# Optimization experiments

Hardware: AMD Instinct MI355X
Metric: run time of the kernel (lower is better)

The kernel has to match this reference:

```python
import jax, jax.numpy as jnp
import numpy as np

B, S, E = 1, 2048, 4096
H, D = 32, 128  # num_heads, head_dim


def setup_inputs() -> dict:
    key = jax.random.key(0)
    k1, k2, k3 = jax.random.split(key, 3)
    hidden_states = jax.random.normal(k1, (B, S, E), dtype=jnp.float32)
    # real RoPE tables (half-rotation / llama-style), base 10000
    inv_freq = 1.0 / (10000.0 ** (np.arange(0, D, 2, dtype=np.float32) / D))  # [D/2]
    pos = np.arange(S, dtype=np.float32)
    freqs = np.outer(pos, inv_freq)                      # [S, D/2]
    emb = np.concatenate([freqs, freqs], axis=-1)        # [S, D]
    cos = jnp.asarray(np.cos(emb), dtype=jnp.float32)
    sin = jnp.asarray(np.sin(emb), dtype=jnp.float32)
    w_pack = jax.random.normal(k2, (3 * E, E), dtype=jnp.float32) * (E ** -0.5)
    w_o = jax.random.normal(k3, (E, E), dtype=jnp.float32) * (E ** -0.5)
    return {"hidden_states": hidden_states, "cos": cos, "sin": sin,
            "w_pack": w_pack, "w_o": w_o}


def _rotate_half(x):
    x1, x2 = jnp.split(x, 2, axis=-1)
    return jnp.concatenate([-x2, x1], axis=-1)


def reference(hidden_states, cos, sin, w_pack, w_o):
    # fused QKV projection (W_pack, no bias)
    qkv = jnp.einsum('bse,fe->bsf', hidden_states, w_pack)      # [B,S,3E]
    q, k, v = jnp.split(qkv, 3, axis=-1)
    q = q.reshape(B, S, H, D)
    k = k.reshape(B, S, H, D)
    v = v.reshape(B, S, H, D)
    # RoPE (7B path; is_13b=False)
    c = cos[None, :, None, :]
    s = sin[None, :, None, :]
    q = q * c + _rotate_half(q) * s
    k = k * c + _rotate_half(k) * s
    # causal attention (prefill, empty past KV cache)
    scale = 1.0 / jnp.sqrt(jnp.asarray(D, dtype=q.dtype))
    scores = jnp.einsum('bqhd,bkhd->bhqk', q, k) * scale        # [B,H,S,S]
    causal = jnp.tril(jnp.ones((S, S), dtype=bool))
    scores = jnp.where(causal[None, None], scores, jnp.asarray(-1e30, scores.dtype))
    probs = jax.nn.softmax(scores, axis=-1)
    attn = jnp.einsum('bhqk,bkhd->bqhd', probs, v)              # [B,S,H,D]
    attn = attn.reshape(B, S, H * D)
    # output projection
    return jnp.einsum('bsf,ef->bse', attn, w_o)
```

## Files before the change

### kernel.cpp

```cpp
#include <hip/hip_runtime.h>

typedef unsigned short u16;
typedef unsigned int   u32;
typedef __attribute__((ext_vector_type(8))) short short8;
typedef __attribute__((ext_vector_type(4))) float f32x4;

__device__ __forceinline__ float b2f(u16 u) {
  union { float f; u32 i; } v; v.i = ((u32)u) << 16; return v.f;
}
__device__ __forceinline__ u16 f2b(float f) {
  union { float f; u32 i; } v; v.f = f;
  u32 r = v.i + 0x7fffu + ((v.i >> 16) & 1u);
  return (u16)(r >> 16);
}

__device__ __forceinline__ void gload_lds16(const void* g, void* l) {
  __builtin_amdgcn_global_load_lds(
      (const __attribute__((address_space(1))) void*)g,
      (__attribute__((address_space(3))) void*)l, 16, 0, 0);
}

template <int N> __device__ __forceinline__ void wait_vmcnt() {
  if constexpr (N == 0)      asm volatile("s_waitcnt vmcnt(0)" ::: "memory");
  else if constexpr (N == 2) asm volatile("s_waitcnt vmcnt(2)" ::: "memory");
  else if constexpr (N == 3) asm volatile("s_waitcnt vmcnt(3)" ::: "memory");
  else if constexpr (N == 6) asm volatile("s_waitcnt vmcnt(6)" ::: "memory");
  else if constexpr (N == 8) asm volatile("s_waitcnt vmcnt(8)" ::: "memory");
  else static_assert(N < 0, "unsupported vmcnt literal");
}

__device__ __forceinline__ ushort4 cvt4(float4 v) {
  ushort4 o;
  o.x = f2b(v.x); o.y = f2b(v.y); o.z = f2b(v.z); o.w = f2b(v.w);
  return o;
}

__global__ __launch_bounds__(256) void cvt_all(const float* __restrict__ hs,
                                               const float* __restrict__ wp,
                                               const float* __restrict__ wo,
                                               u16* __restrict__ h_bf,
                                               u16* __restrict__ wp_bf,
                                               u16* __restrict__ wo_bf) {
  const long H4 = 2097152, W4 = 12582912, O4 = 4194304;
  for (long i = (long)blockIdx.x * 256 + threadIdx.x; i < H4 + W4 + O4;
       i += (long)gridDim.x * 256) {
    if (i < H4)
      ((ushort4*)h_bf)[i] = cvt4(((const float4*)hs)[i]);
    else if (i < H4 + W4)
      ((ushort4*)wp_bf)[i - H4] = cvt4(((const float4*)wp)[i - H4]);
    else
      ((ushort4*)wo_bf)[i - H4 - W4] = cvt4(((const float4*)wo)[i - H4 - W4]);
  }
}

__device__ __forceinline__ short8 frag_ld64(const u16* base, int rbase, int kk,
                                            int fr, int fq) {
  const int r = rbase + fr;
  return *(const short8*)(base + r * 64 + ((((kk << 2) + fq) ^ (r & 7)) << 3));
}

__global__ __launch_bounds__(512, 2) void gemm8p(const u16* __restrict__ A,
                                                 const u16* __restrict__ B,
                                                 u16* __restrict__ Cq,
                                                 u16* __restrict__ VT,
                                                 int M, int N, int K) {
  constexpr int AE = 16384;
  constexpr int BUFSZ = AE + 12288;
  __shared__ u16 lds[2 * BUFSZ];
  const int tid = threadIdx.x;
  const int wid = tid >> 6, lane = tid & 63;
  const int fr = lane & 15, fq = lane >> 4;
  const int mA = (wid >> 2) * 128;
  const int nB = (wid & 3) * 48;

  const int nty = M >> 8;
  const int qx = gridDim.x >> 3;
  const int wg = (blockIdx.x & 7) * qx + (blockIdx.x >> 3);
  const int by = wg % nty, bx = wg / nty;
  const long row0 = (long)by * 256, col0 = (long)bx * 192;

  const int rr8 = tid >> 3;
  const int jl = (tid & 7) ^ (rr8 & 7);
  const u16* gA = A + (row0 + rr8) * (long)K + jl * 8;
  const u16* gB = B + (col0 + rr8) * (long)K + jl * 8;

  f32x4 acc[8][3];
#pragma unroll
  for (int m = 0; m < 8; ++m)
#pragma unroll
    for (int n = 0; n < 3; ++n) acc[m][n] = f32x4{0.f, 0.f, 0.f, 0.f};

  const int NT = K >> 6;

  auto stageA = [&](int i, int t) {
    gload_lds16(gA + (long)(i * 64) * K + (long)t * 64,
                lds + (t & 1) * BUFSZ + (i * 512 + tid) * 8);
  };
  auto stageB = [&](int i, int t) {
    gload_lds16(gB + (long)(i * 64) * K + (long)t * 64,
                lds + (t & 1) * BUFSZ + AE + (i * 512 + tid) * 8);
  };

#pragma unroll
  for (int i = 0; i < 4; ++i) stageA(i, 0);
#pragma unroll
  for (int i = 0; i < 3; ++i) stageB(i, 0);
#pragma unroll
  for (int i = 0; i < 3; ++i) stageB(i, 1);
  wait_vmcnt<3>();
  __builtin_amdgcn_s_barrier();

  for (int t = 0; t < NT; ++t) {
    const u16* SA = lds + (t & 1) * BUFSZ;
    const u16* SB = SA + AE;
    short8 a0[4], a1[4], b0[3], b1[3];

#pragma unroll
    for (int m = 0; m < 4; ++m) a0[m] = frag_ld64(SA, mA + m * 16, 0, fr, fq);
#pragma unroll
    for (int n = 0; n < 3; ++n) b0[n] = frag_ld64(SB, nB + n * 16, 0, fr, fq);
#pragma unroll
    for (int n = 0; n < 3; ++n) b1[n] = frag_ld64(SB, nB + n * 16, 1, fr, fq);
    if (t + 1 < NT) { stageA(0, t + 1); stageA(1, t + 1); }
    __builtin_amdgcn_s_setprio(1);
#pragma unroll
    for (int m = 0; m < 4; ++m)
#pragma unroll
      for (int n = 0; n < 3; ++n)
        acc[m][n] = __builtin_amdgcn_mfma_f32_16x16x32_bf16(a0[m], b0[n], acc[m][n], 0, 0, 0);
    __builtin_amdgcn_s_setprio(0);
    asm volatile("s_waitcnt lgkmcnt(0)" ::: "memory");
    __builtin_amdgcn_s_barrier();

#pragma unroll
    for (int m = 0; m < 4; ++m) a1[m] = frag_ld64(SA, mA + 64 + m * 16, 0, fr, fq);
    if (t + 1 < NT) { stageA(2, t + 1); stageA(3, t + 1); }
    __builtin_amdgcn_s_setprio(1);
#pragma unroll
    for (int m = 0; m < 4; ++m)
#pragma unroll
      for (int n = 0; n < 3; ++n)
        acc[4 + m][n] = __builtin_amdgcn_mfma_f32_16x16x32_bf16(a1[m], b0[n], acc[4 + m][n], 0, 0, 0);
    __builtin_amdgcn_s_setprio(0);
    __builtin_amdgcn_s_barrier();

#pragma unroll
    for (int m = 0; m < 4; ++m) a0[m] = frag_ld64(SA, mA + m * 16, 1, fr, fq);
    if (t + 2 < NT) { stageB(0, t + 2); stageB(1, t + 2); }
    __builtin_amdgcn_s_setprio(1);
#pragma unroll
    for (int m = 0; m < 4; ++m)
#pragma unroll
      for (int n = 0; n < 3; ++n)
        acc[m][n] = __builtin_amdgcn_mfma_f32_16x16x32_bf16(a0[m], b1[n], acc[m][n], 0, 0, 0);
    __builtin_amdgcn_s_setprio(0);
    __builtin_amdgcn_s_barrier();

#pragma unroll
    for (int m = 0; m < 4; ++m) a1[m] = frag_ld64(SA, mA + 64 + m * 16, 1, fr, fq);
    if (t + 2 < NT) stageB(2, t + 2);
    __builtin_amdgcn_s_setprio(1);
#pragma unroll
    for (int m = 0; m < 4; ++m)
#pragma unroll
      for (int n = 0; n < 3; ++n)
        acc[4 + m][n] = __builtin_amdgcn_mfma_f32_16x16x32_bf16(a1[m], b1[n], acc[4 + m][n], 0, 0, 0);
    __builtin_amdgcn_s_setprio(0);
    if (t + 2 < NT) wait_vmcnt<3>();
    else            wait_vmcnt<0>();
    __builtin_amdgcn_s_barrier();
  }

#pragma unroll
  for (int m = 0; m < 8; ++m)
#pragma unroll
    for (int n = 0; n < 3; ++n) {
      const long c = col0 + nB + n * 16 + fr;
      const long rb = row0 + mA + m * 16 + fq * 4;
      if (c >= 8192) {
        ushort4 o;
        o.x = f2b(acc[m][n][0]); o.y = f2b(acc[m][n][1]);
        o.z = f2b(acc[m][n][2]); o.w = f2b(acc[m][n][3]);
        *(ushort4*)(VT + (c - 8192) * 2048 + rb) = o;
      } else {
#pragma unroll
        for (int j = 0; j < 4; ++j) Cq[(rb + j) * N + c] = f2b(acc[m][n][j]);
      }
    }
}

__global__ __launch_bounds__(512, 2) void gemm2_4p(const u16* __restrict__ A,
                                                   const u16* __restrict__ B,
                                                   float* __restrict__ C,
                                                   int M, int N, int K) {
  constexpr int AE = 16384;
  constexpr int BUFSZ = AE + 8192;
  __shared__ u16 lds[2 * BUFSZ];
  const int tid = threadIdx.x;
  const int wid = tid >> 6, lane = tid & 63;
  const int fr = lane & 15, fq = lane >> 4;
  const int mA = (wid >> 2) * 128;
  const int nB = (wid & 3) * 32;

  const int nty = M >> 8;
  const int qx = gridDim.x >> 3;
  const int wg = (blockIdx.x & 7) * qx + (blockIdx.x >> 3);
  const int by = wg % nty, bx = wg / nty;
  const long row0 = (long)by * 256, col0 = (long)bx * 128;

  const int rr8 = tid >> 3;
  const int jl = (tid & 7) ^ (rr8 & 7);
  const u16* gA = A + (row0 + rr8) * (long)K + jl * 8;
  const u16* gB = B + (col0 + rr8) * (long)K + jl * 8;

  f32x4 acc[8][2];
#pragma unroll
  for (int m = 0; m < 8; ++m)
#pragma unroll
    for (int n = 0; n < 2; ++n) acc[m][n] = f32x4{0.f, 0.f, 0.f, 0.f};

  const int NT = K >> 6;

  auto stageA = [&](int i, int t) {
    gload_lds16(gA + (long)(i * 64) * K + (long)t * 64,
                lds + (t & 1) * BUFSZ + (i * 512 + tid) * 8);
  };
  auto stageB = [&](int i, int t) {
    gload_lds16(gB + (long)(i * 64) * K + (long)t * 64,
                lds + (t & 1) * BUFSZ + AE + (i * 512 + tid) * 8);
  };

#pragma unroll
  for (int i = 0; i < 4; ++i) stageA(i, 0);
#pragma unroll
  for (int i = 0; i < 2; ++i) stageB(i, 0);
#pragma unroll
  for (int i = 0; i < 2; ++i) stageB(i, 1);
  wait_vmcnt<2>();
  __builtin_amdgcn_s_barrier();

  for (int t = 0; t < NT; ++t) {
    const u16* SA = lds + (t & 1) * BUFSZ;
    const u16* SB = SA + AE;
    short8 a0[4], a1[4], b0[2], b1[2];

#pragma unroll
    for (int m = 0; m < 4; ++m) a0[m] = frag_ld64(SA, mA + m * 16, 0, fr, fq);
#pragma unroll
    for (int n = 0; n < 2; ++n) b0[n] = frag_ld64(SB, nB + n * 16, 0, fr, fq);
#pragma unroll
    for (int n = 0; n < 2; ++n) b1[n] = frag_ld64(SB, nB + n * 16, 1, fr, fq);
    if (t + 1 < NT) { stageA(0, t + 1); stageA(1, t + 1); }
    __builtin_amdgcn_s_setprio(1);
#pragma unroll
    for (int m = 0; m < 4; ++m)
#pragma unroll
      for (int n = 0; n < 2; ++n)
        acc[m][n] = __builtin_amdgcn_mfma_f32_16x16x32_bf16(a0[m], b0[n], acc[m][n], 0, 0, 0);
    __builtin_amdgcn_s_setprio(0);
    asm volatile("s_waitcnt lgkmcnt(0)" ::: "memory");
    __builtin_amdgcn_s_barrier();

#pragma unroll
    for (int m = 0; m < 4; ++m) a1[m] = frag_ld64(SA, mA + 64 + m * 16, 0, fr, fq);
    if (t + 1 < NT) { stageA(2, t + 1); stageA(3, t + 1); }
    __builtin_amdgcn_s_setprio(1);
#pragma unroll
    for (int m = 0; m < 4; ++m)
#pragma unroll
      for (int n = 0; n < 2; ++n)
        acc[4 + m][n] = __builtin_amdgcn_mfma_f32_16x16x32_bf16(a1[m], b0[n], acc[4 + m][n], 0, 0, 0);
    __builtin_amdgcn_s_setprio(0);
    __builtin_amdgcn_s_barrier();

#pragma unroll
    for (int m = 0; m < 4; ++m) a0[m] = frag_ld64(SA, mA + m * 16, 1, fr, fq);
    if (t + 2 < NT) stageB(0, t + 2);
    __builtin_amdgcn_s_setprio(1);
#pragma unroll
    for (int m = 0; m < 4; ++m)
#pragma unroll
      for (int n = 0; n < 2; ++n)
        acc[m][n] = __builtin_amdgcn_mfma_f32_16x16x32_bf16(a0[m], b1[n], acc[m][n], 0, 0, 0);
    __builtin_amdgcn_s_setprio(0);
    __builtin_amdgcn_s_barrier();

#pragma unroll
    for (int m = 0; m < 4; ++m) a1[m] = frag_ld64(SA, mA + 64 + m * 16, 1, fr, fq);
    if (t + 2 < NT) stageB(1, t + 2);
    __builtin_amdgcn_s_setprio(1);
#pragma unroll
    for (int m = 0; m < 4; ++m)
#pragma unroll
      for (int n = 0; n < 2; ++n)
        acc[4 + m][n] = __builtin_amdgcn_mfma_f32_16x16x32_bf16(a1[m], b1[n], acc[4 + m][n], 0, 0, 0);
    __builtin_amdgcn_s_setprio(0);
    if (t + 2 < NT) wait_vmcnt<2>();
    else            wait_vmcnt<0>();
    __builtin_amdgcn_s_barrier();
  }

#pragma unroll
  for (int m = 0; m < 8; ++m)
#pragma unroll
    for (int n = 0; n < 2; ++n)
#pragma unroll
      for (int j = 0; j < 4; ++j) {
        const long r = row0 + mA + m * 16 + fq * 4 + j;
        const long c = col0 + nB + n * 16 + fr;
        C[r * N + c] = acc[m][n][j];
      }
}

__global__ __launch_bounds__(256) void rope_qk(u16* __restrict__ qkv,
                                               const float* __restrict__ cosb,
                                               const float* __restrict__ sinb) {
  const int idx = blockIdx.x * 256 + threadIdx.x;
  const int dq  = idx & 15;
  const int h   = (idx >> 4) & 31;
  const int seg = (idx >> 9) & 1;
  const int s   = idx >> 10;
  const int d0  = dq * 4;
  u16* base = qkv + (long)s * 12288 + seg * 4096 + h * 128;
  const ushort4 x1 = *(const ushort4*)(base + d0);
  const ushort4 x2 = *(const ushort4*)(base + d0 + 64);
  const float4 c1 = *(const float4*)(cosb + s * 128 + d0);
  const float4 s1 = *(const float4*)(sinb + s * 128 + d0);
  const float4 c2 = *(const float4*)(cosb + s * 128 + d0 + 64);
  const float4 s2 = *(const float4*)(sinb + s * 128 + d0 + 64);
  const float scale = seg ? 1.0f : 0.08838834764831845f;
  float x1f[4] = {b2f(x1.x), b2f(x1.y), b2f(x1.z), b2f(x1.w)};
  float x2f[4] = {b2f(x2.x), b2f(x2.y), b2f(x2.z), b2f(x2.w)};
  const float c1a[4] = {c1.x, c1.y, c1.z, c1.w}, s1a[4] = {s1.x, s1.y, s1.z, s1.w};
  const float c2a[4] = {c2.x, c2.y, c2.z, c2.w}, s2a[4] = {s2.x, s2.y, s2.z, s2.w};
  ushort4 o1, o2;
  u16* o1p = (u16*)&o1; u16* o2p = (u16*)&o2;
#pragma unroll
  for (int j = 0; j < 4; ++j) {
    o1p[j] = f2b((x1f[j] * c1a[j] - x2f[j] * s1a[j]) * scale);
    o2p[j] = f2b((x2f[j] * c2a[j] + x1f[j] * s2a[j]) * scale);
  }
  *(ushort4*)(base + d0) = o1;
  *(ushort4*)(base + d0 + 64) = o2;
}

__global__ __launch_bounds__(256) void attn_fwd(const u16* __restrict__ Qb,
                                                const u16* __restrict__ Kb,
                                                const u16* __restrict__ Vt,
                                                u16* __restrict__ Ob) {
  const int h = blockIdx.y;
  const int tid = threadIdx.x;
  const int wid = tid >> 6, lane = tid & 63;
  const int fr = lane & 15, fq = lane >> 4;

  __shared__ u16 Ks[3][64 * 128];
  __shared__ u16 Vts[3][128 * 64];
  __shared__ u16 Ps[4][32 * 72];

  auto stage = [&](int t, int buf) {
    const int kv0 = t * 64;
#pragma unroll
    for (int i = 0; i < 4; ++i) {
      const int c = wid * 4 + i;
      {
        const int r = c * 4 + (lane >> 4);
        const int p = lane & 15;
        const int jsrc = p ^ (r & 7);
        gload_lds16(Kb + (long)(kv0 + r) * 12288 + h * 128 + jsrc * 8,
                    (char*)Ks[buf] + c * 1024);
      }
      {
        const int d = c * 8 + (lane >> 3);
        const int p = lane & 7;
        const int jsrc = p ^ (d & 7);
        gload_lds16(Vt + (long)(h * 128 + d) * 2048 + kv0 + jsrc * 8,
                    (char*)Vts[buf] + c * 1024);
      }
    }
  };

#pragma unroll
  for (int pass = 0; pass < 2; ++pass) {
    const int qt = pass == 0 ? (int)blockIdx.x : 15 - (int)blockIdx.x;
    const int q0 = qt * 128;
    const int nt = 2 * qt + 2;
    const int wq_hi = q0 + wid * 32 + 31;

    short8 qf[2][4];
#pragma unroll
    for (int m = 0; m < 2; ++m) {
      const long qrow = q0 + wid * 32 + m * 16 + fr;
#pragma unroll
      for (int kk = 0; kk < 4; ++kk)
        qf[m][kk] = *(const short8*)(Qb + qrow * 12288 + h * 128 + kk * 32 + fq * 8);
    }

    f32x4 Oacc[2][8];
#pragma unroll
    for (int m = 0; m < 2; ++m)
#pragma unroll
      for (int f = 0; f < 8; ++f) Oacc[m][f] = f32x4{0.f, 0.f, 0.f, 0.f};
    float mrun[2][4], lrun[2][4];
#pragma unroll
    for (int m = 0; m < 2; ++m)
#pragma unroll
      for (int j = 0; j < 4; ++j) { mrun[m][j] = -1e30f; lrun[m][j] = 0.f; }

    stage(0, 0);
    if (nt > 1) { stage(1, 1); wait_vmcnt<8>(); }
    else        wait_vmcnt<0>();
    __builtin_amdgcn_s_barrier();

    for (int t = 0; t < nt; ++t) {
      const int cur = t % 3;
      const int kv0 = t * 64;
      if (t + 2 < nt) stage(t + 2, (t + 2) % 3);

      if (kv0 <= wq_hi) {
        f32x4 S[2][4];
#pragma unroll
        for (int m = 0; m < 2; ++m)
#pragma unroll
          for (int n = 0; n < 4; ++n) S[m][n] = f32x4{0.f, 0.f, 0.f, 0.f};
#pragma unroll
        for (int kk = 0; kk < 4; ++kk) {
          short8 kf[4];
#pragma unroll
          for (int n = 0; n < 4; ++n) {
            const int r = n * 16 + fr;
            const int p = (kk * 4 + fq) ^ (r & 7);
            kf[n] = *(const short8*)((const char*)Ks[cur] + r * 256 + p * 16);
          }
#pragma unroll
          for (int m = 0; m < 2; ++m)
#pragma unroll
            for (int n = 0; n < 4; ++n)
              S[m][n] = __builtin_amdgcn_mfma_f32_16x16x32_bf16(qf[m][kk], kf[n], S[m][n], 0, 0, 0);
        }

        float P[2][4][4];
#pragma unroll
        for (int m = 0; m < 2; ++m) {
          float tm[4] = {-1e30f, -1e30f, -1e30f, -1e30f};
#pragma unroll
          for (int n = 0; n < 4; ++n) {
            const int kv = kv0 + n * 16 + fr;
#pragma unroll
            for (int j = 0; j < 4; ++j) {
              const int qi = q0 + wid * 32 + m * 16 + fq * 4 + j;
              const float s = (kv <= qi) ? S[m][n][j] : -1e30f;
              P[m][n][j] = s;
              tm[j] = fmaxf(tm[j], s);
            }
          }
#pragma unroll
          for (int j = 0; j < 4; ++j)
#pragma unroll
            for (int msk = 1; msk < 16; msk <<= 1)
              tm[j] = fmaxf(tm[j], __shfl_xor(tm[j], msk));

          float al[4], rs[4];
#pragma unroll
          for (int j = 0; j < 4; ++j) {
            const float mn = fmaxf(mrun[m][j], tm[j]);
            al[j] = __expf(mrun[m][j] - mn);
            mrun[m][j] = mn;
            rs[j] = 0.f;
          }
#pragma unroll
          for (int n = 0; n < 4; ++n)
#pragma unroll
            for (int j = 0; j < 4; ++j) {
              const float p = __expf(P[m][n][j] - mrun[m][j]);
              P[m][n][j] = p;
              rs[j] += p;
            }
#pragma unroll
          for (int j = 0; j < 4; ++j) {
#pragma unroll
            for (int msk = 1; msk < 16; msk <<= 1) rs[j] += __shfl_xor(rs[j], msk);
            lrun[m][j] = lrun[m][j] * al[j] + rs[j];
          }
#pragma unroll
          for (int f = 0; f < 8; ++f) {
            f32x4 o = Oacc[m][f];
#pragma unroll
            for (int j = 0; j < 4; ++j) o[j] *= al[j];
            Oacc[m][f] = o;
          }
        }

#pragma unroll
        for (int m = 0; m < 2; ++m)
#pragma unroll
          for (int n = 0; n < 4; ++n)
#pragma unroll
            for (int j = 0; j < 4; ++j)
              Ps[wid][(m * 16 + fq * 4 + j) * 72 + n * 16 + fr] = f2b(P[m][n][j]);

#pragma unroll
        for (int kb = 0; kb < 2; ++kb) {
          short8 pa0 = *(const short8*)(Ps[wid] + (fr) * 72 + kb * 32 + fq * 8);
          short8 pa1 = *(const short8*)(Ps[wid] + (16 + fr) * 72 + kb * 32 + fq * 8);
#pragma unroll
          for (int f = 0; f < 8; ++f) {
            const int d = f * 16 + fr;
            const int p = (kb * 4 + fq) ^ (d & 7);
            short8 vf = *(const short8*)((const char*)Vts[cur] + d * 128 + p * 16);
            Oacc[0][f] = __builtin_amdgcn_mfma_f32_16x16x32_bf16(pa0, vf, Oacc[0][f], 0, 0, 0);
            Oacc[1][f] = __builtin_amdgcn_mfma_f32_16x16x32_bf16(pa1, vf, Oacc[1][f], 0, 0, 0);
          }
        }
      }
      if (t + 2 < nt) wait_vmcnt<8>();
      else            wait_vmcnt<0>();
      __builtin_amdgcn_s_barrier();
    }

#pragma unroll
    for (int m = 0; m < 2; ++m)
#pragma unroll
      for (int j = 0; j < 4; ++j) {
        const float inv = 1.f / lrun[m][j];
        const long r = q0 + wid * 32 + m * 16 + fq * 4 + j;
#pragma unroll
        for (int f = 0; f < 8; ++f)
          Ob[r * 4096 + h * 128 + f * 16 + fr] = f2b(Oacc[m][f][j] * inv);
      }
  }
}

extern "C" void kernel_launch(void* const* d_in, const int* in_sizes, int n_in,
                              void* d_out, int out_size, void* d_ws, size_t ws_size,
                              hipStream_t stream) {
  const float* hs   = (const float*)d_in[0];
  const float* cosb = (const float*)d_in[1];
  const float* sinb = (const float*)d_in[2];
  const float* wp   = (const float*)d_in[3];
  const float* wo   = (const float*)d_in[4];
  float* out = (float*)d_out;
  char* ws = (char*)d_ws;

  u16* h_bf  = (u16*)(ws);
  u16* attn  = (u16*)(ws);
  u16* wp_bf = (u16*)(ws + 16777216);
  u16* wo_bf = (u16*)(ws + 117440512);
  u16* qkv   = (u16*)(ws + 150994944);
  u16* vt    = (u16*)(ws + 201326592);

  cvt_all<<<4096, 256, 0, stream>>>(hs, wp, wo, h_bf, wp_bf, wo_bf);
  gemm8p<<<512, 512, 0, stream>>>(h_bf, wp_bf, qkv, vt, 2048, 12288, 4096);
  rope_qk<<<8192, 256, 0, stream>>>(qkv, cosb, sinb);
  attn_fwd<<<dim3(8, 32), 256, 0, stream>>>(qkv, qkv + 4096, vt, attn);
  gemm2_4p<<<256, 512, 0, stream>>>(attn, wo_bf, out, 2048, 4096, 4096);
}
```

Baseline: 467.1 us.

## Process two adjacent query tiles per 512-thread attention block with shared K/V staging

The attention kernel moves from 4 waves running two load-balanced q-tile passes one after another to 8 waves in two groups. Each group handles one of two adjacent q-tiles at the same time, and both groups share the same K/V LDS tiles. This halves K/V staging traffic per tile and raises waves per CU for latency hiding. In exchange the per-block work now grows with blockIdx.x, so the old pair balancing (tile i with tile 15-i) is lost. The pipeline also drops from triple to double buffering with a full vmcnt(0) wait on every step, which shortens the prefetch distance.

```diff
diff --git a/kernel.cpp b/kernel.cpp
--- a/kernel.cpp
+++ b/kernel.cpp
@@ -25,7 +25,6 @@
   else if constexpr (N == 2) asm volatile("s_waitcnt vmcnt(2)" ::: "memory");
   else if constexpr (N == 3) asm volatile("s_waitcnt vmcnt(3)" ::: "memory");
   else if constexpr (N == 6) asm volatile("s_waitcnt vmcnt(6)" ::: "memory");
-  else if constexpr (N == 8) asm volatile("s_waitcnt vmcnt(8)" ::: "memory");
   else static_assert(N < 0, "unsupported vmcnt literal");
 }
 
@@ -344,24 +343,26 @@
   *(ushort4*)(base + d0 + 64) = o2;
 }
 
-__global__ __launch_bounds__(256) void attn_fwd(const u16* __restrict__ Qb,
-                                                const u16* __restrict__ Kb,
-                                                const u16* __restrict__ Vt,
-                                                u16* __restrict__ Ob) {
+__global__ __launch_bounds__(512, 2) void attn_fwd(const u16* __restrict__ Qb,
+                                                   const u16* __restrict__ Kb,
+                                                   const u16* __restrict__ Vt,
+                                                   u16* __restrict__ Ob) {
   const int h = blockIdx.y;
   const int tid = threadIdx.x;
   const int wid = tid >> 6, lane = tid & 63;
+  const int grp = wid >> 2;
+  const int w4 = wid & 3;
   const int fr = lane & 15, fq = lane >> 4;
 
-  __shared__ u16 Ks[3][64 * 128];
-  __shared__ u16 Vts[3][128 * 64];
-  __shared__ u16 Ps[4][32 * 72];
+  __shared__ u16 Ks[2][64 * 128];
+  __shared__ u16 Vts[2][128 * 64];
+  __shared__ u16 Ps[8][32 * 72];
 
   auto stage = [&](int t, int buf) {
     const int kv0 = t * 64;
 #pragma unroll
-    for (int i = 0; i < 4; ++i) {
-      const int c = wid * 4 + i;
+    for (int i = 0; i < 2; ++i) {
+      const int c = wid * 2 + i;
       {
         const int r = c * 4 + (lane >> 4);
         const int p = lane & 15;
@@ -379,155 +380,150 @@
     }
   };
 
-#pragma unroll
-  for (int pass = 0; pass < 2; ++pass) {
-    const int qt = pass == 0 ? (int)blockIdx.x : 15 - (int)blockIdx.x;
-    const int q0 = qt * 128;
-    const int nt = 2 * qt + 2;
-    const int wq_hi = q0 + wid * 32 + 31;
-
-    short8 qf[2][4];
-#pragma unroll
-    for (int m = 0; m < 2; ++m) {
-      const long qrow = q0 + wid * 32 + m * 16 + fr;
-#pragma unroll
-      for (int kk = 0; kk < 4; ++kk)
-        qf[m][kk] = *(const short8*)(Qb + qrow * 12288 + h * 128 + kk * 32 + fq * 8);
-    }
-
-    f32x4 Oacc[2][8];
-#pragma unroll
-    for (int m = 0; m < 2; ++m)
-#pragma unroll
-      for (int f = 0; f < 8; ++f) Oacc[m][f] = f32x4{0.f, 0.f, 0.f, 0.f};
-    float mrun[2][4], lrun[2][4];
-#pragma unroll
-    for (int m = 0; m < 2; ++m)
-#pragma unroll
-      for (int j = 0; j < 4; ++j) { mrun[m][j] = -1e30f; lrun[m][j] = 0.f; }
-
-    stage(0, 0);
-    if (nt > 1) { stage(1, 1); wait_vmcnt<8>(); }
-    else        wait_vmcnt<0>();
-    __builtin_amdgcn_s_barrier();
-
-    for (int t = 0; t < nt; ++t) {
-      const int cur = t % 3;
-      const int kv0 = t * 64;
-      if (t + 2 < nt) stage(t + 2, (t + 2) % 3);
-
-      if (kv0 <= wq_hi) {
-        f32x4 S[2][4];
+  const int qt = 2 * (int)blockIdx.x + (grp ^ 1);
+  const int q0 = qt * 128;
+  const int nt = 4 * (int)blockIdx.x + 4;
+  const int wq_hi = q0 + w4 * 32 + 31;
+
+  short8 qf[2][4];
+#pragma unroll
+  for (int m = 0; m < 2; ++m) {
+    const long qrow = q0 + w4 * 32 + m * 16 + fr;
+#pragma unroll
+    for (int kk = 0; kk < 4; ++kk)
+      qf[m][kk] = *(const short8*)(Qb + qrow * 12288 + h * 128 + kk * 32 + fq * 8);
+  }
+
+  f32x4 Oacc[2][8];
+#pragma unroll
+  for (int m = 0; m < 2; ++m)
+#pragma unroll
+    for (int f = 0; f < 8; ++f) Oacc[m][f] = f32x4{0.f, 0.f, 0.f, 0.f};
+  float mrun[2][4], lrun[2][4];
+#pragma unroll
+  for (int m = 0; m < 2; ++m)
+#pragma unroll
+    for (int j = 0; j < 4; ++j) { mrun[m][j] = -1e30f; lrun[m][j] = 0.f; }
+
+  stage(0, 0);
+  wait_vmcnt<0>();
+  __builtin_amdgcn_s_barrier();
+
+  for (int t = 0; t < nt; ++t) {
+    const int cur = t & 1;
+    const int kv0 = t * 64;
+    if (t + 1 < nt) stage(t + 1, cur ^ 1);
+
+    if (kv0 <= wq_hi) {
+      f32x4 S[2][4];
+#pragma unroll
+      for (int m = 0; m < 2; ++m)
+#pragma unroll
+        for (int n = 0; n < 4; ++n) S[m][n] = f32x4{0.f, 0.f, 0.f, 0.f};
+#pragma unroll
+      for (int kk = 0; kk < 4; ++kk) {
+        short8 kf[4];
+#pragma unroll
+        for (int n = 0; n < 4; ++n) {
+          const int r = n * 16 + fr;
+          const int p = (kk * 4 + fq) ^ (r & 7);
+          kf[n] = *(const short8*)((const char*)Ks[cur] + r * 256 + p * 16);
+        }
 #pragma unroll
         for (int m = 0; m < 2; ++m)
 #pragma unroll
-          for (int n = 0; n < 4; ++n) S[m][n] = f32x4{0.f, 0.f, 0.f, 0.f};
-#pragma unroll
-        for (int kk = 0; kk < 4; ++kk) {
-          short8 kf[4];
-#pragma unroll
-          for (int n = 0; n < 4; ++n) {
-            const int r = n * 16 + fr;
-            const int p = (kk * 4 + fq) ^ (r & 7);
-            kf[n] = *(const short8*)((const char*)Ks[cur] + r * 256 + p * 16);
-          }
-#pragma unroll
-          for (int m = 0; m < 2; ++m)
-#pragma unroll
-            for (int n = 0; n < 4; ++n)
-              S[m][n] = __builtin_amdgcn_mfma_f32_16x16x32_bf16(qf[m][kk], kf[n], S[m][n], 0, 0, 0);
-        }
-
-        float P[2][4][4];
-#pragma unroll
-        for (int m = 0; m < 2; ++m) {
-          float tm[4] = {-1e30f, -1e30f, -1e30f, -1e30f};
-#pragma unroll
-          for (int n = 0; n < 4; ++n) {
-            const int kv = kv0 + n * 16 + fr;
-#pragma unroll
-            for (int j = 0; j < 4; ++j) {
-              const int qi = q0 + wid * 32 + m * 16 + fq * 4 + j;
-              const float s = (kv <= qi) ? S[m][n][j] : -1e30f;
-              P[m][n][j] = s;
-              tm[j] = fmaxf(tm[j], s);
-            }
-          }
-#pragma unroll
-          for (int j = 0; j < 4; ++j)
-#pragma unroll
-            for (int msk = 1; msk < 16; msk <<= 1)
-              tm[j] = fmaxf(tm[j], __shfl_xor(tm[j], msk));
-
-          float al[4], rs[4];
+          for (int n = 0; n < 4; ++n)
+            S[m][n] = __builtin_amdgcn_mfma_f32_16x16x32_bf16(qf[m][kk], kf[n], S[m][n], 0, 0, 0);
+      }
+
+      float P[2][4][4];
+#pragma unroll
+      for (int m = 0; m < 2; ++m) {
+        float tm[4] = {-1e30f, -1e30f, -1e30f, -1e30f};
+#pragma unroll
+        for (int n = 0; n < 4; ++n) {
+          const int kv = kv0 + n * 16 + fr;
 #pragma unroll
           for (int j = 0; j < 4; ++j) {
-            const float mn = fmaxf(mrun[m][j], tm[j]);
-            al[j] = __expf(mrun[m][j] - mn);
-            mrun[m][j] = mn;
-            rs[j] = 0.f;
-          }
-#pragma unroll
-          for (int n = 0; n < 4; ++n)
-#pragma unroll
-            for (int j = 0; j < 4; ++j) {
-              const float p = __expf(P[m][n][j] - mrun[m][j]);
-              P[m][n][j] = p;
-              rs[j] += p;
-            }
-#pragma unroll
-          for (int j = 0; j < 4; ++j) {
-#pragma unroll
-            for (int msk = 1; msk < 16; msk <<= 1) rs[j] += __shfl_xor(rs[j], msk);
-            lrun[m][j] = lrun[m][j] * al[j] + rs[j];
-          }
-#pragma unroll
-          for (int f = 0; f < 8; ++f) {
-            f32x4 o = Oacc[m][f];
-#pragma unroll
-            for (int j = 0; j < 4; ++j) o[j] *= al[j];
-            Oacc[m][f] = o;
+            const int qi = q0 + w4 * 32 + m * 16 + fq * 4 + j;
+            const float s = (kv <= qi) ? S[m][n][j] : -1e30f;
+            P[m][n][j] = s;
+            tm[j] = fmaxf(tm[j], s);
           }
         }
-
-#pragma unroll
-        for (int m = 0; m < 2; ++m)
-#pragma unroll
-          for (int n = 0; n < 4; ++n)
-#pragma unroll
-            for (int j = 0; j < 4; ++j)
-              Ps[wid][(m * 16 + fq * 4 + j) * 72 + n * 16 + fr] = f2b(P[m][n][j]);
-
-#pragma unroll
-        for (int kb = 0; kb < 2; ++kb) {
-          short8 pa0 = *(const short8*)(Ps[wid] + (fr) * 72 + kb * 32 + fq * 8);
-          short8 pa1 = *(const short8*)(Ps[wid] + (16 + fr) * 72 + kb * 32 + fq * 8);
-#pragma unroll
-          for (int f = 0; f < 8; ++f) {
-            const int d = f * 16 + fr;
-            const int p = (kb * 4 + fq) ^ (d & 7);
-            short8 vf = *(const short8*)((const char*)Vts[cur] + d * 128 + p * 16);
-            Oacc[0][f] = __builtin_amdgcn_mfma_f32_16x16x32_bf16(pa0, vf, Oacc[0][f], 0, 0, 0);
-            Oacc[1][f] = __builtin_amdgcn_mfma_f32_16x16x32_bf16(pa1, vf, Oacc[1][f], 0, 0, 0);
+#pragma unroll
+        for (int j = 0; j < 4; ++j)
+#pragma unroll
+          for (int msk = 1; msk < 16; msk <<= 1)
+            tm[j] = fmaxf(tm[j], __shfl_xor(tm[j], msk));
+
+        float al[4], rs[4];
+#pragma unroll
+        for (int j = 0; j < 4; ++j) {
+          const float mn = fmaxf(mrun[m][j], tm[j]);
+          al[j] = __expf(mrun[m][j] - mn);
+          mrun[m][j] = mn;
+          rs[j] = 0.f;
+        }
+#pragma unroll
+        for (int n = 0; n < 4; ++n)
+#pragma unroll
+          for (int j = 0; j < 4; ++j) {
+            const float p = __expf(P[m][n][j] - mrun[m][j]);
+            P[m][n][j] = p;
+            rs[j] += p;
           }
+#pragma unroll
+        for (int j = 0; j < 4; ++j) {
+#pragma unroll
+          for (int msk = 1; msk < 16; msk <<= 1) rs[j] += __shfl_xor(rs[j], msk);
+          lrun[m][j] = lrun[m][j] * al[j] + rs[j];
         }
-      }
-      if (t + 2 < nt) wait_vmcnt<8>();
-      else            wait_vmcnt<0>();
-      __builtin_amdgcn_s_barrier();
+#pragma unroll
+        for (int f = 0; f < 8; ++f) {
+          f32x4 o = Oacc[m][f];
+#pragma unroll
+          for (int j = 0; j < 4; ++j) o[j] *= al[j];
+          Oacc[m][f] = o;
+        }
+      }
+
+#pragma unroll
+      for (int m = 0; m < 2; ++m)
+#pragma unroll
+        for (int n = 0; n < 4; ++n)
+#pragma unroll
+          for (int j = 0; j < 4; ++j)
+            Ps[wid][(m * 16 + fq * 4 + j) * 72 + n * 16 + fr] = f2b(P[m][n][j]);
+
+#pragma unroll
+      for (int kb = 0; kb < 2; ++kb) {
+        short8 pa0 = *(const short8*)(Ps[wid] + (fr) * 72 + kb * 32 + fq * 8);
+        short8 pa1 = *(const short8*)(Ps[wid] + (16 + fr) * 72 + kb * 32 + fq * 8);
+#pragma unroll
+        for (int f = 0; f < 8; ++f) {
+          const int d = f * 16 + fr;
+          const int p = (kb * 4 + fq) ^ (d & 7);
+          short8 vf = *(const short8*)((const char*)Vts[cur] + d * 128 + p * 16);
+          Oacc[0][f] = __builtin_amdgcn_mfma_f32_16x16x32_bf16(pa0, vf, Oacc[0][f], 0, 0, 0);
+          Oacc[1][f] = __builtin_amdgcn_mfma_f32_16x16x32_bf16(pa1, vf, Oacc[1][f], 0, 0, 0);
+        }
+      }
     }
-
-#pragma unroll
-    for (int m = 0; m < 2; ++m)
-#pragma unroll
-      for (int j = 0; j < 4; ++j) {
-        const float inv = 1.f / lrun[m][j];
-        const long r = q0 + wid * 32 + m * 16 + fq * 4 + j;
-#pragma unroll
-        for (int f = 0; f < 8; ++f)
-          Ob[r * 4096 + h * 128 + f * 16 + fr] = f2b(Oacc[m][f][j] * inv);
-      }
+    wait_vmcnt<0>();
+    __builtin_amdgcn_s_barrier();
   }
+
+#pragma unroll
+  for (int m = 0; m < 2; ++m)
+#pragma unroll
+    for (int j = 0; j < 4; ++j) {
+      const float inv = 1.f / lrun[m][j];
+      const long r = q0 + w4 * 32 + m * 16 + fq * 4 + j;
+#pragma unroll
+      for (int f = 0; f < 8; ++f)
+        Ob[r * 4096 + h * 128 + f * 16 + fr] = f2b(Oacc[m][f][j] * inv);
+    }
 }
 
 extern "C" void kernel_launch(void* const* d_in, const int* in_sizes, int n_in,
@@ -551,6 +547,6 @@
   cvt_all<<<4096, 256, 0, stream>>>(hs, wp, wo, h_bf, wp_bf, wo_bf);
   gemm8p<<<512, 512, 0, stream>>>(h_bf, wp_bf, qkv, vt, 2048, 12288, 4096);
   rope_qk<<<8192, 256, 0, stream>>>(qkv, cosb, sinb);
-  attn_fwd<<<dim3(8, 32), 256, 0, stream>>>(qkv, qkv + 4096, vt, attn);
+  attn_fwd<<<dim3(8, 32), 512, 0, stream>>>(qkv, qkv + 4096, vt, attn);
   gemm2_4p<<<256, 512, 0, stream>>>(attn, wo_bf, out, 2048, 4096, 4096);
 }
```

Measured after the change: 469.4 us. No clear change (+0.5%).
